# Kernel tuning notes

Hardware: AMD Instinct MI355X
Metric: run time of the kernel (lower is better)

Reference implementation:

```python
import jax, jax.numpy as jnp
from jax import lax
import numpy as np

DN = ('NHWC', 'HWIO', 'NHWC')


def setup_inputs() -> dict:
    key = jax.random.key(0)
    ks = jax.random.split(key, 4)
    B, T, H, W, Cin, Cout, K = 4, 16, 64, 64, 32, 64, 3
    x = jax.random.normal(ks[0], (B, T, H, W, Cin), dtype=jnp.float32)
    kernel = jax.random.normal(ks[1], (K, K, Cin, 4 * Cout), dtype=jnp.float32) * 0.05
    rec_kernel = jax.random.normal(ks[2], (K, K, Cout, 4 * Cout), dtype=jnp.float32) * 0.05
    bias = jnp.zeros((4 * Cout,), dtype=jnp.float32)
    gamma = jnp.ones((Cout,), dtype=jnp.float32)
    beta = jnp.zeros((Cout,), dtype=jnp.float32)
    moving_mean = jnp.zeros((Cout,), dtype=jnp.float32)
    moving_var = jnp.ones((Cout,), dtype=jnp.float32)
    return dict(x=x, kernel=kernel, rec_kernel=rec_kernel, bias=bias,
                gamma=gamma, beta=beta, moving_mean=moving_mean, moving_var=moving_var)


def _hard_sigmoid(z):
    # Keras hard_sigmoid: clip(0.2*x + 0.5, 0, 1)
    return jnp.clip(0.2 * z + 0.5, 0.0, 1.0)


def _conv(x, w):
    return lax.conv_general_dilated(x, w, (1, 1), 'SAME', dimension_numbers=DN)


def reference(x, kernel, rec_kernel, bias, gamma, beta, moving_mean, moving_var):
    B, T, H, W, Cin = x.shape
    Cout = rec_kernel.shape[2]
    # Precompute input-to-gate convs for all timesteps at once: (B*T,H,W,4C)
    gx = _conv(x.reshape(B * T, H, W, Cin), kernel) + bias
    gx = gx.reshape(B, T, H, W, 4 * Cout).transpose(1, 0, 2, 3, 4)  # (T,B,H,W,4C)

    def step(carry, gxt):
        h, c = carry
        g = gxt + _conv(h, rec_kernel)  # (B,H,W,4C)
        i, f, cc, o = jnp.split(g, 4, axis=-1)  # Keras gate order i,f,c,o
        i = _hard_sigmoid(i)
        f = _hard_sigmoid(f)
        c = f * c + i * jnp.tanh(cc)
        h = _hard_sigmoid(o) * jnp.tanh(c)
        return (h, c), h

    h0 = jnp.zeros((B, H, W, Cout), dtype=x.dtype)
    c0 = jnp.zeros((B, H, W, Cout), dtype=x.dtype)
    _, hs = lax.scan(step, (h0, c0), gx)  # (T,B,H,W,C)
    y = hs.transpose(1, 0, 2, 3, 4)  # (B,T,H,W,C)
    # BatchNorm, inference mode (training=False), eps=1e-3
    inv = gamma * lax.rsqrt(moving_var + 1e-3)
    return y * inv + (beta - moving_mean * inv)
```

## Files before the change

kernel.cpp:

```cpp
#include <hip/hip_runtime.h>
#include <math.h>

#define B_ 4
#define T_ 16
#define H_ 64
#define W_ 64
#define CIN 32
#define CO 64
#define NG 256
#define PXS 40

typedef __attribute__((ext_vector_type(8))) short bf16x8;
typedef __attribute__((ext_vector_type(4))) float f32x4;

__device__ __forceinline__ float hsig(float z) {
    return fminf(1.f, fmaxf(0.f, 0.2f * z + 0.5f));
}

__device__ __forceinline__ float ftanh(float x) {
    float e = __builtin_amdgcn_exp2f(x * 2.8853900817779268f);
    return 1.f - 2.f * __builtin_amdgcn_rcpf(e + 1.f);
}

__device__ __forceinline__ unsigned short f2bf(float f) {
    union { float f; unsigned u; } v; v.f = f;
    unsigned r = v.u + 0x7FFFu + ((v.u >> 16) & 1u);
    return (unsigned short)(r >> 16);
}

__global__ void transform_weights(const float* __restrict__ wk,
                                  const float* __restrict__ wr,
                                  unsigned short* __restrict__ wkT,
                                  unsigned short* __restrict__ wrT)
{
    int i = blockIdx.x * 256 + threadIdx.x;
    if (i < 9 * 256 * 32) {
        int k = i & 31, n = (i >> 5) & 255, kpos = i >> 13;
        wkT[i] = f2bf(wk[(kpos * 32 + k) * 256 + n]);
    }
    if (i < 9 * 2 * 256 * 32) {
        int k = i & 31, n = (i >> 5) & 255, q = (i >> 13) & 1, kpos = i >> 14;
        wrT[i] = f2bf(wr[(kpos * 64 + q * 32 + k) * 256 + n]);
    }
}

template<bool FIRST>
__global__ __launch_bounds__(512, 2)
void convlstm_step(const float* __restrict__ x,
                   const unsigned short* __restrict__ wkT,
                   const unsigned short* __restrict__ wrT,
                   const float* __restrict__ bias,
                   const float* __restrict__ gamma,
                   const float* __restrict__ beta,
                   const float* __restrict__ mean,
                   const float* __restrict__ var,
                   const unsigned short* __restrict__ hin,
                   unsigned short* __restrict__ hout,
                   float* __restrict__ cbuf,
                   float* __restrict__ out,
                   int t)
{
    __shared__ __align__(16) unsigned short sx[6 * 18 * PXS];
    __shared__ __align__(16) unsigned short sh[2][6 * 18 * PXS];
    __shared__ __align__(16) float axx[4 * 4 * 4 * 16 * 20];

    const int tid = threadIdx.x;
    const int wv = tid >> 6, lane = tid & 63;
    const int ln = lane & 15, kg = lane >> 4;
    const bool hwave = (wv < 4);
    const int sl = wv & 3;

    const int bi = blockIdx.x;
    const int b = bi >> 6, tile = bi & 63;
    const int oy = (tile >> 2) * 4;
    const int ox = (tile & 3) * 16;

    if (!hwave) {
#pragma unroll
        for (int i = 0; i < 2; ++i) {
            int e = (tid - 256) + i * 256;
            if (e < 432) {
                int c8 = e & 3, p = e >> 2;
                int row = p / 18, col = p - row * 18;
                int gy = oy - 1 + row, gx = ox - 1 + col;
                float4 v0 = make_float4(0.f, 0.f, 0.f, 0.f), v1 = v0;
                if ((unsigned)gy < (unsigned)H_ && (unsigned)gx < (unsigned)W_) {
                    const float* p32 = &x[((((size_t)b * T_ + t) * H_ + gy) * W_ + gx) * CIN + c8 * 8];
                    v0 = *(const float4*)p32; v1 = *(const float4*)(p32 + 4);
                }
                unsigned short* d = &sx[(row * 18 + col) * PXS + c8 * 8];
                d[0] = f2bf(v0.x); d[1] = f2bf(v0.y); d[2] = f2bf(v0.z); d[3] = f2bf(v0.w);
                d[4] = f2bf(v1.x); d[5] = f2bf(v1.y); d[6] = f2bf(v1.z); d[7] = f2bf(v1.w);
            }
        }
    } else if (!FIRST) {
#pragma unroll
        for (int i = 0; i < 4; ++i) {
            int e = tid + i * 256;
            if (e < 864) {
                int o = e & 7, p = e >> 3;
                int row = p / 18, col = p - row * 18;
                int gy = oy - 1 + row, gx = ox - 1 + col;
                uint4 v = make_uint4(0u, 0u, 0u, 0u);
                if ((unsigned)gy < (unsigned)H_ && (unsigned)gx < (unsigned)W_)
                    v = *(const uint4*)&hin[(((size_t)b * H_ + gy) * W_ + gx) * CO + o * 8];
                int q = o >> 2, s4 = o & 3;
                *(uint4*)&sh[q][(row * 18 + col) * PXS + s4 * 8] = v;
            }
        }
    }
    __syncthreads();

    f32x4 acc[4][4];
#pragma unroll
    for (int g = 0; g < 4; ++g)
#pragma unroll
        for (int r = 0; r < 4; ++r) acc[g][r] = (f32x4){0.f, 0.f, 0.f, 0.f};

    const int nbase = sl * 16 + ln;

    if (!hwave) {
        const unsigned short* wkp = wkT + (size_t)nbase * 32 + kg * 8;
        bf16x8 bx[4];
#pragma unroll
        for (int g = 0; g < 4; ++g)
            bx[g] = *(const bf16x8*)(wkp + (size_t)(g * 64) * 32);
#pragma unroll
        for (int kpos = 0; kpos < 9; ++kpos) {
            const int ky = kpos / 3, kx = kpos - ky * 3;
            bf16x8 nbx[4];
            if (kpos < 8) {
#pragma unroll
                for (int g = 0; g < 4; ++g)
                    nbx[g] = *(const bf16x8*)(wkp + (size_t)((kpos + 1) * 256 + g * 64) * 32);
            }
            bf16x8 a[4];
#pragma unroll
            for (int r = 0; r < 4; ++r)
                a[r] = *(const bf16x8*)&sx[((r + ky) * 18 + ln + kx) * PXS + kg * 8];
#pragma unroll
            for (int g = 0; g < 4; ++g)
#pragma unroll
                for (int r = 0; r < 4; ++r)
                    acc[g][r] = __builtin_amdgcn_mfma_f32_16x16x32_bf16(a[r], bx[g], acc[g][r], 0, 0, 0);
            if (kpos < 8) {
#pragma unroll
                for (int g = 0; g < 4; ++g) bx[g] = nbx[g];
            }
        }
    } else if (!FIRST) {
        const unsigned short* wrp = wrT + (size_t)nbase * 32 + kg * 8;
        bf16x8 bh[2][4];
#pragma unroll
        for (int q = 0; q < 2; ++q)
#pragma unroll
            for (int g = 0; g < 4; ++g)
                bh[q][g] = *(const bf16x8*)(wrp + (size_t)(q * 256 + g * 64) * 32);
#pragma unroll
        for (int kpos = 0; kpos < 9; ++kpos) {
            const int ky = kpos / 3, kx = kpos - ky * 3;
            bf16x8 nbh[2][4];
            if (kpos < 8) {
#pragma unroll
                for (int q = 0; q < 2; ++q)
#pragma unroll
                    for (int g = 0; g < 4; ++g)
                        nbh[q][g] = *(const bf16x8*)(wrp + (size_t)(((kpos + 1) * 2 + q) * 256 + g * 64) * 32);
            }
#pragma unroll
            for (int q = 0; q < 2; ++q) {
                bf16x8 a[4];
#pragma unroll
                for (int r = 0; r < 4; ++r)
                    a[r] = *(const bf16x8*)&sh[q][((r + ky) * 18 + ln + kx) * PXS + kg * 8];
#pragma unroll
                for (int g = 0; g < 4; ++g)
#pragma unroll
                    for (int r = 0; r < 4; ++r)
                        acc[g][r] = __builtin_amdgcn_mfma_f32_16x16x32_bf16(a[r], bh[q][g], acc[g][r], 0, 0, 0);
            }
            if (kpos < 8) {
#pragma unroll
                for (int q = 0; q < 2; ++q)
#pragma unroll
                    for (int g = 0; g < 4; ++g) bh[q][g] = nbh[q][g];
            }
        }
    }

    if (!hwave) {
#pragma unroll
        for (int g = 0; g < 4; ++g)
#pragma unroll
            for (int r = 0; r < 4; ++r)
                *(f32x4*)&axx[((((sl * 4 + g) * 4 + r) * 16) + ln) * 20 + kg * 4] = acc[g][r];
    }
    __syncthreads();
    if (!hwave) return;

#pragma unroll
    for (int g = 0; g < 4; ++g)
#pragma unroll
        for (int r = 0; r < 4; ++r) {
            f32x4 v = *(const f32x4*)&axx[((((sl * 4 + g) * 4 + r) * 16) + ln) * 20 + kg * 4];
            acc[g][r] += v;
        }

    const int ch = sl * 16 + ln;
    const float bi0 = bias[ch], bi1 = bias[64 + ch], bi2 = bias[128 + ch], bi3 = bias[192 + ch];
    const float inv = gamma[ch] * rsqrtf(var[ch] + 1e-3f);
    const float shift = beta[ch] - mean[ch] * inv;

    float cprev[4][4];
    if (!FIRST) {
#pragma unroll
        for (int r = 0; r < 4; ++r)
#pragma unroll
            for (int reg = 0; reg < 4; ++reg) {
                size_t pix = ((size_t)b * H_ + oy + r) * W_ + (ox + kg * 4 + reg);
                cprev[r][reg] = cbuf[pix * CO + ch];
            }
    } else {
#pragma unroll
        for (int r = 0; r < 4; ++r)
#pragma unroll
            for (int reg = 0; reg < 4; ++reg) cprev[r][reg] = 0.f;
    }

#pragma unroll
    for (int r = 0; r < 4; ++r) {
        const int gy = oy + r;
#pragma unroll
        for (int reg = 0; reg < 4; ++reg) {
            const int gx = ox + kg * 4 + reg;
            size_t pix = ((size_t)b * H_ + gy) * W_ + gx;
            float ig = hsig(acc[0][r][reg] + bi0);
            float fg = hsig(acc[1][r][reg] + bi1);
            float cg = ftanh(acc[2][r][reg] + bi2);
            float og = hsig(acc[3][r][reg] + bi3);
            float cv = fg * cprev[r][reg] + ig * cg;
            float hv = og * ftanh(cv);
            cbuf[pix * CO + ch] = cv;
            hout[pix * CO + ch] = f2bf(hv);
            out[((((size_t)b * T_ + t) * H_ + gy) * W_ + gx) * CO + ch] = hv * inv + shift;
        }
    }
}

extern "C" void kernel_launch(void* const* d_in, const int* in_sizes, int n_in,
                              void* d_out, int out_size, void* d_ws, size_t ws_size,
                              hipStream_t stream)
{
    (void)in_sizes; (void)n_in; (void)out_size; (void)ws_size;
    const float* x     = (const float*)d_in[0];
    const float* wk    = (const float*)d_in[1];
    const float* wr    = (const float*)d_in[2];
    const float* bias  = (const float*)d_in[3];
    const float* gamma = (const float*)d_in[4];
    const float* beta  = (const float*)d_in[5];
    const float* mean  = (const float*)d_in[6];
    const float* var   = (const float*)d_in[7];
    float* out = (float*)d_out;

    const size_t plane = (size_t)B_ * H_ * W_ * CO;
    unsigned short* h0 = (unsigned short*)d_ws;
    unsigned short* h1 = h0 + plane;
    float* cb = (float*)(h1 + plane);
    unsigned short* wkT = (unsigned short*)(cb + plane);
    unsigned short* wrT = wkT + 9 * 256 * 32;

    transform_weights<<<576, 256, 0, stream>>>(wk, wr, wkT, wrT);

    for (int t = 0; t < T_; ++t) {
        const unsigned short* hin = (t & 1) ? h0 : h1;
        unsigned short* houtp     = (t & 1) ? h1 : h0;
        if (t == 0)
            convlstm_step<true><<<256, 512, 0, stream>>>(x, wkT, wrT, bias, gamma, beta, mean, var,
                                                         hin, houtp, cb, out, t);
        else
            convlstm_step<false><<<256, 512, 0, stream>>>(x, wkT, wrT, bias, gamma, beta, mean, var,
                                                          hin, houtp, cb, out, t);
    }
}
```

Baseline: 308.8 us.

## Rebalance MFMA work between x-wave and h-wave, prefetch cell state, nontemporal stores

The recurrent conv's second channel half is split across the two wave groups: the x-conv waves now also handle kernel positions 0-4 of the h-conv's second 32-channel half, and the h-waves keep positions 5-8. This evens out MFMA counts between the waves so they reach the barrier at about the same time. Bias, batchnorm params and the previous cell state are now loaded before the MFMA loop so their latency is hidden behind compute. MFMA blocks are wrapped in s_setprio, and the c and output stores become nontemporal, which trades cache residency of cbuf for reduced write traffic.

```diff
diff --git a/kernel.cpp b/kernel.cpp
--- a/kernel.cpp
+++ b/kernel.cpp
@@ -111,79 +111,145 @@
     }
     __syncthreads();
 
+    const int nbase = sl * 16 + ln;
+    const int ch = nbase;
+
+    float bi0 = 0.f, bi1 = 0.f, bi2 = 0.f, bi3 = 0.f, inv = 0.f, shift = 0.f;
+    float cprev[4][4];
+    if (hwave) {
+        bi0 = bias[ch]; bi1 = bias[64 + ch]; bi2 = bias[128 + ch]; bi3 = bias[192 + ch];
+        inv = gamma[ch] * rsqrtf(var[ch] + 1e-3f);
+        shift = beta[ch] - mean[ch] * inv;
+        if (!FIRST) {
+#pragma unroll
+            for (int r = 0; r < 4; ++r)
+#pragma unroll
+                for (int reg = 0; reg < 4; ++reg) {
+                    size_t pix = ((size_t)b * H_ + oy + r) * W_ + (ox + kg * 4 + reg);
+                    cprev[r][reg] = cbuf[pix * CO + ch];
+                }
+        } else {
+#pragma unroll
+            for (int r = 0; r < 4; ++r)
+#pragma unroll
+                for (int reg = 0; reg < 4; ++reg) cprev[r][reg] = 0.f;
+        }
+    }
+
     f32x4 acc[4][4];
 #pragma unroll
     for (int g = 0; g < 4; ++g)
 #pragma unroll
         for (int r = 0; r < 4; ++r) acc[g][r] = (f32x4){0.f, 0.f, 0.f, 0.f};
-
-    const int nbase = sl * 16 + ln;
 
     if (!hwave) {
         const unsigned short* wkp = wkT + (size_t)nbase * 32 + kg * 8;
-        bf16x8 bx[4];
+        const unsigned short* wrp = wrT + (size_t)nbase * 32 + kg * 8;
+        bf16x8 bx[4], bq[4];
 #pragma unroll
         for (int g = 0; g < 4; ++g)
             bx[g] = *(const bf16x8*)(wkp + (size_t)(g * 64) * 32);
+        if (!FIRST) {
+#pragma unroll
+            for (int g = 0; g < 4; ++g)
+                bq[g] = *(const bf16x8*)(wrp + (size_t)(1 * 256 + g * 64) * 32);
+        }
 #pragma unroll
         for (int kpos = 0; kpos < 9; ++kpos) {
             const int ky = kpos / 3, kx = kpos - ky * 3;
-            bf16x8 nbx[4];
+            bf16x8 nbx[4], nbq[4];
             if (kpos < 8) {
 #pragma unroll
                 for (int g = 0; g < 4; ++g)
                     nbx[g] = *(const bf16x8*)(wkp + (size_t)((kpos + 1) * 256 + g * 64) * 32);
             }
+            if (!FIRST && kpos < 4) {
+#pragma unroll
+                for (int g = 0; g < 4; ++g)
+                    nbq[g] = *(const bf16x8*)(wrp + (size_t)(((kpos + 1) * 2 + 1) * 256 + g * 64) * 32);
+            }
             bf16x8 a[4];
 #pragma unroll
             for (int r = 0; r < 4; ++r)
                 a[r] = *(const bf16x8*)&sx[((r + ky) * 18 + ln + kx) * PXS + kg * 8];
+            __builtin_amdgcn_s_setprio(1);
 #pragma unroll
             for (int g = 0; g < 4; ++g)
 #pragma unroll
                 for (int r = 0; r < 4; ++r)
                     acc[g][r] = __builtin_amdgcn_mfma_f32_16x16x32_bf16(a[r], bx[g], acc[g][r], 0, 0, 0);
+            __builtin_amdgcn_s_setprio(0);
+            if (!FIRST && kpos < 5) {
+#pragma unroll
+                for (int r = 0; r < 4; ++r)
+                    a[r] = *(const bf16x8*)&sh[1][((r + ky) * 18 + ln + kx) * PXS + kg * 8];
+                __builtin_amdgcn_s_setprio(1);
+#pragma unroll
+                for (int g = 0; g < 4; ++g)
+#pragma unroll
+                    for (int r = 0; r < 4; ++r)
+                        acc[g][r] = __builtin_amdgcn_mfma_f32_16x16x32_bf16(a[r], bq[g], acc[g][r], 0, 0, 0);
+                __builtin_amdgcn_s_setprio(0);
+            }
             if (kpos < 8) {
 #pragma unroll
                 for (int g = 0; g < 4; ++g) bx[g] = nbx[g];
+            }
+            if (!FIRST && kpos < 4) {
+#pragma unroll
+                for (int g = 0; g < 4; ++g) bq[g] = nbq[g];
             }
         }
     } else if (!FIRST) {
         const unsigned short* wrp = wrT + (size_t)nbase * 32 + kg * 8;
-        bf16x8 bh[2][4];
-#pragma unroll
-        for (int q = 0; q < 2; ++q)
-#pragma unroll
-            for (int g = 0; g < 4; ++g)
-                bh[q][g] = *(const bf16x8*)(wrp + (size_t)(q * 256 + g * 64) * 32);
+        bf16x8 bq0[4], bq1[4];
+#pragma unroll
+        for (int g = 0; g < 4; ++g)
+            bq0[g] = *(const bf16x8*)(wrp + (size_t)(g * 64) * 32);
 #pragma unroll
         for (int kpos = 0; kpos < 9; ++kpos) {
             const int ky = kpos / 3, kx = kpos - ky * 3;
-            bf16x8 nbh[2][4];
+            bf16x8 nbq0[4], nbq1[4];
             if (kpos < 8) {
 #pragma unroll
-                for (int q = 0; q < 2; ++q)
-#pragma unroll
-                    for (int g = 0; g < 4; ++g)
-                        nbh[q][g] = *(const bf16x8*)(wrp + (size_t)(((kpos + 1) * 2 + q) * 256 + g * 64) * 32);
-            }
-#pragma unroll
-            for (int q = 0; q < 2; ++q) {
-                bf16x8 a[4];
+                for (int g = 0; g < 4; ++g)
+                    nbq0[g] = *(const bf16x8*)(wrp + (size_t)((kpos + 1) * 2 * 256 + g * 64) * 32);
+            }
+            if (kpos >= 4 && kpos < 8) {
+#pragma unroll
+                for (int g = 0; g < 4; ++g)
+                    nbq1[g] = *(const bf16x8*)(wrp + (size_t)(((kpos + 1) * 2 + 1) * 256 + g * 64) * 32);
+            }
+            bf16x8 a[4];
+#pragma unroll
+            for (int r = 0; r < 4; ++r)
+                a[r] = *(const bf16x8*)&sh[0][((r + ky) * 18 + ln + kx) * PXS + kg * 8];
+            __builtin_amdgcn_s_setprio(1);
+#pragma unroll
+            for (int g = 0; g < 4; ++g)
 #pragma unroll
                 for (int r = 0; r < 4; ++r)
-                    a[r] = *(const bf16x8*)&sh[q][((r + ky) * 18 + ln + kx) * PXS + kg * 8];
+                    acc[g][r] = __builtin_amdgcn_mfma_f32_16x16x32_bf16(a[r], bq0[g], acc[g][r], 0, 0, 0);
+            __builtin_amdgcn_s_setprio(0);
+            if (kpos >= 5) {
+#pragma unroll
+                for (int r = 0; r < 4; ++r)
+                    a[r] = *(const bf16x8*)&sh[1][((r + ky) * 18 + ln + kx) * PXS + kg * 8];
+                __builtin_amdgcn_s_setprio(1);
 #pragma unroll
                 for (int g = 0; g < 4; ++g)
 #pragma unroll
                     for (int r = 0; r < 4; ++r)
-                        acc[g][r] = __builtin_amdgcn_mfma_f32_16x16x32_bf16(a[r], bh[q][g], acc[g][r], 0, 0, 0);
+                        acc[g][r] = __builtin_amdgcn_mfma_f32_16x16x32_bf16(a[r], bq1[g], acc[g][r], 0, 0, 0);
+                __builtin_amdgcn_s_setprio(0);
             }
             if (kpos < 8) {
 #pragma unroll
-                for (int q = 0; q < 2; ++q)
-#pragma unroll
-                    for (int g = 0; g < 4; ++g) bh[q][g] = nbh[q][g];
+                for (int g = 0; g < 4; ++g) bq0[g] = nbq0[g];
+            }
+            if (kpos >= 4 && kpos < 8) {
+#pragma unroll
+                for (int g = 0; g < 4; ++g) bq1[g] = nbq1[g];
             }
         }
     }
@@ -205,27 +271,6 @@
             f32x4 v = *(const f32x4*)&axx[((((sl * 4 + g) * 4 + r) * 16) + ln) * 20 + kg * 4];
             acc[g][r] += v;
         }
-
-    const int ch = sl * 16 + ln;
-    const float bi0 = bias[ch], bi1 = bias[64 + ch], bi2 = bias[128 + ch], bi3 = bias[192 + ch];
-    const float inv = gamma[ch] * rsqrtf(var[ch] + 1e-3f);
-    const float shift = beta[ch] - mean[ch] * inv;
-
-    float cprev[4][4];
-    if (!FIRST) {
-#pragma unroll
-        for (int r = 0; r < 4; ++r)
-#pragma unroll
-            for (int reg = 0; reg < 4; ++reg) {
-                size_t pix = ((size_t)b * H_ + oy + r) * W_ + (ox + kg * 4 + reg);
-                cprev[r][reg] = cbuf[pix * CO + ch];
-            }
-    } else {
-#pragma unroll
-        for (int r = 0; r < 4; ++r)
-#pragma unroll
-            for (int reg = 0; reg < 4; ++reg) cprev[r][reg] = 0.f;
-    }
 
 #pragma unroll
     for (int r = 0; r < 4; ++r) {
@@ -240,9 +285,10 @@
             float og = hsig(acc[3][r][reg] + bi3);
             float cv = fg * cprev[r][reg] + ig * cg;
             float hv = og * ftanh(cv);
-            cbuf[pix * CO + ch] = cv;
+            __builtin_nontemporal_store(cv, &cbuf[pix * CO + ch]);
             hout[pix * CO + ch] = f2bf(hv);
-            out[((((size_t)b * T_ + t) * H_ + gy) * W_ + gx) * CO + ch] = hv * inv + shift;
+            __builtin_nontemporal_store(hv * inv + shift,
+                &out[((((size_t)b * T_ + t) * H_ + gy) * W_ + gx) * CO + ch]);
         }
     }
 }
```

New measurement: 288.5 us. -6.6%, faster.

## Balance MFMA work between x and h waves and split gate epilogue

Applied to the files above, without the earlier changes.

Rebalances the convolution work so the x-wave also takes part of the recurrent conv (second channel half), giving 14 vs 13 chunks instead of 9 vs 18. Both waves now exchange partial sums through LDS and each runs the gate epilogue for half the rows, so no wave idles after the barrier. Weight loads use a deeper 3-ahead register pipeline, MFMA blocks are wrapped in s_setprio, and the c-state and output stores are nontemporal. The cost is higher register pressure from the deeper pipeline, and the h-wave now depends on partial sums from the x-wave for every row.

```diff
diff --git a/kernel.cpp b/kernel.cpp
--- a/kernel.cpp
+++ b/kernel.cpp
@@ -109,140 +109,137 @@
             }
         }
     }
-    __syncthreads();
-
-    f32x4 acc[4][4];
-#pragma unroll
-    for (int g = 0; g < 4; ++g)
-#pragma unroll
-        for (int r = 0; r < 4; ++r) acc[g][r] = (f32x4){0.f, 0.f, 0.f, 0.f};
 
     const int nbase = sl * 16 + ln;
-
-    if (!hwave) {
-        const unsigned short* wkp = wkT + (size_t)nbase * 32 + kg * 8;
-        bf16x8 bx[4];
-#pragma unroll
-        for (int g = 0; g < 4; ++g)
-            bx[g] = *(const bf16x8*)(wkp + (size_t)(g * 64) * 32);
-#pragma unroll
-        for (int kpos = 0; kpos < 9; ++kpos) {
-            const int ky = kpos / 3, kx = kpos - ky * 3;
-            bf16x8 nbx[4];
-            if (kpos < 8) {
-#pragma unroll
-                for (int g = 0; g < 4; ++g)
-                    nbx[g] = *(const bf16x8*)(wkp + (size_t)((kpos + 1) * 256 + g * 64) * 32);
-            }
-            bf16x8 a[4];
-#pragma unroll
-            for (int r = 0; r < 4; ++r)
-                a[r] = *(const bf16x8*)&sx[((r + ky) * 18 + ln + kx) * PXS + kg * 8];
-#pragma unroll
-            for (int g = 0; g < 4; ++g)
-#pragma unroll
-                for (int r = 0; r < 4; ++r)
-                    acc[g][r] = __builtin_amdgcn_mfma_f32_16x16x32_bf16(a[r], bx[g], acc[g][r], 0, 0, 0);
-            if (kpos < 8) {
-#pragma unroll
-                for (int g = 0; g < 4; ++g) bx[g] = nbx[g];
-            }
-        }
-    } else if (!FIRST) {
-        const unsigned short* wrp = wrT + (size_t)nbase * 32 + kg * 8;
-        bf16x8 bh[2][4];
-#pragma unroll
-        for (int q = 0; q < 2; ++q)
-#pragma unroll
-            for (int g = 0; g < 4; ++g)
-                bh[q][g] = *(const bf16x8*)(wrp + (size_t)(q * 256 + g * 64) * 32);
-#pragma unroll
-        for (int kpos = 0; kpos < 9; ++kpos) {
-            const int ky = kpos / 3, kx = kpos - ky * 3;
-            bf16x8 nbh[2][4];
-            if (kpos < 8) {
-#pragma unroll
-                for (int q = 0; q < 2; ++q)
-#pragma unroll
-                    for (int g = 0; g < 4; ++g)
-                        nbh[q][g] = *(const bf16x8*)(wrp + (size_t)(((kpos + 1) * 2 + q) * 256 + g * 64) * 32);
-            }
-#pragma unroll
-            for (int q = 0; q < 2; ++q) {
-                bf16x8 a[4];
-#pragma unroll
-                for (int r = 0; r < 4; ++r)
-                    a[r] = *(const bf16x8*)&sh[q][((r + ky) * 18 + ln + kx) * PXS + kg * 8];
-#pragma unroll
-                for (int g = 0; g < 4; ++g)
-#pragma unroll
-                    for (int r = 0; r < 4; ++r)
-                        acc[g][r] = __builtin_amdgcn_mfma_f32_16x16x32_bf16(a[r], bh[q][g], acc[g][r], 0, 0, 0);
-            }
-            if (kpos < 8) {
-#pragma unroll
-                for (int q = 0; q < 2; ++q)
-#pragma unroll
-                    for (int g = 0; g < 4; ++g) bh[q][g] = nbh[q][g];
-            }
-        }
-    }
-
-    if (!hwave) {
-#pragma unroll
-        for (int g = 0; g < 4; ++g)
-#pragma unroll
-            for (int r = 0; r < 4; ++r)
-                *(f32x4*)&axx[((((sl * 4 + g) * 4 + r) * 16) + ln) * 20 + kg * 4] = acc[g][r];
-    }
-    __syncthreads();
-    if (!hwave) return;
-
-#pragma unroll
-    for (int g = 0; g < 4; ++g)
-#pragma unroll
-        for (int r = 0; r < 4; ++r) {
-            f32x4 v = *(const f32x4*)&axx[((((sl * 4 + g) * 4 + r) * 16) + ln) * 20 + kg * 4];
-            acc[g][r] += v;
-        }
-
-    const int ch = sl * 16 + ln;
+    const int ch = nbase;
+    const unsigned short* wkp = wkT + (size_t)nbase * 32 + kg * 8;
+    const unsigned short* wrp = wrT + (size_t)nbase * 32 + kg * 8;
+
+    const int rbase = hwave ? 0 : 2;
     const float bi0 = bias[ch], bi1 = bias[64 + ch], bi2 = bias[128 + ch], bi3 = bias[192 + ch];
     const float inv = gamma[ch] * rsqrtf(var[ch] + 1e-3f);
     const float shift = beta[ch] - mean[ch] * inv;
-
-    float cprev[4][4];
+    float cprev[2][4];
     if (!FIRST) {
 #pragma unroll
-        for (int r = 0; r < 4; ++r)
+        for (int rr = 0; rr < 2; ++rr)
 #pragma unroll
             for (int reg = 0; reg < 4; ++reg) {
-                size_t pix = ((size_t)b * H_ + oy + r) * W_ + (ox + kg * 4 + reg);
-                cprev[r][reg] = cbuf[pix * CO + ch];
+                size_t pix = ((size_t)b * H_ + oy + rbase + rr) * W_ + (ox + kg * 4 + reg);
+                cprev[rr][reg] = cbuf[pix * CO + ch];
             }
     } else {
 #pragma unroll
-        for (int r = 0; r < 4; ++r)
-#pragma unroll
-            for (int reg = 0; reg < 4; ++reg) cprev[r][reg] = 0.f;
-    }
-
-#pragma unroll
-    for (int r = 0; r < 4; ++r) {
+        for (int rr = 0; rr < 2; ++rr)
+#pragma unroll
+            for (int reg = 0; reg < 4; ++reg) cprev[rr][reg] = 0.f;
+    }
+
+    __syncthreads();
+
+    f32x4 acc[4][4];
+#pragma unroll
+    for (int g = 0; g < 4; ++g)
+#pragma unroll
+        for (int r = 0; r < 4; ++r) acc[g][r] = (f32x4){0.f, 0.f, 0.f, 0.f};
+
+#define LOADW_X(dst, i) {                                                        \
+    const unsigned short* wp_ = (i < 9) ? (wkp + (size_t)(i) * 8192)             \
+                                        : (wrp + (size_t)(((i) - 9) * 2 + 1) * 8192); \
+    dst[0] = *(const bf16x8*)(wp_);                                              \
+    dst[1] = *(const bf16x8*)(wp_ + 2048);                                       \
+    dst[2] = *(const bf16x8*)(wp_ + 4096);                                       \
+    dst[3] = *(const bf16x8*)(wp_ + 6144); }
+#define LOADW_H(dst, i) {                                                        \
+    const unsigned short* wp_ = (i < 9) ? (wrp + (size_t)((i) * 2) * 8192)       \
+                                        : (wrp + (size_t)(((i) - 4) * 2 + 1) * 8192); \
+    dst[0] = *(const bf16x8*)(wp_);                                              \
+    dst[1] = *(const bf16x8*)(wp_ + 2048);                                       \
+    dst[2] = *(const bf16x8*)(wp_ + 4096);                                       \
+    dst[3] = *(const bf16x8*)(wp_ + 6144); }
+
+    if (!hwave) {
+        constexpr int NC = FIRST ? 9 : 14;
+        bf16x8 pipe[4][4];
+#pragma unroll
+        for (int i = 0; i < 3; ++i) { if (i < NC) LOADW_X(pipe[i], i); }
+#pragma unroll
+        for (int i = 0; i < NC; ++i) {
+            if (i + 3 < NC) LOADW_X(pipe[(i + 3) & 3], (i + 3));
+            const int kq = (i < 9) ? i : i - 9;
+            const int ky = kq / 3, kx = kq - ky * 3;
+            const unsigned short* sb = (i < 9) ? sx : sh[1];
+            bf16x8 a[4];
+#pragma unroll
+            for (int r = 0; r < 4; ++r)
+                a[r] = *(const bf16x8*)&sb[((r + ky) * 18 + ln + kx) * PXS + kg * 8];
+            __builtin_amdgcn_s_setprio(1);
+#pragma unroll
+            for (int g = 0; g < 4; ++g)
+#pragma unroll
+                for (int r = 0; r < 4; ++r)
+                    acc[g][r] = __builtin_amdgcn_mfma_f32_16x16x32_bf16(a[r], pipe[i & 3][g], acc[g][r], 0, 0, 0);
+            __builtin_amdgcn_s_setprio(0);
+        }
+    } else if (!FIRST) {
+        constexpr int NC = 13;
+        bf16x8 pipe[4][4];
+#pragma unroll
+        for (int i = 0; i < 3; ++i) { LOADW_H(pipe[i], i); }
+#pragma unroll
+        for (int i = 0; i < NC; ++i) {
+            if (i + 3 < NC) LOADW_H(pipe[(i + 3) & 3], (i + 3));
+            const int kq = (i < 9) ? i : i - 4;
+            const int ky = kq / 3, kx = kq - ky * 3;
+            const unsigned short* sb = (i < 9) ? sh[0] : sh[1];
+            bf16x8 a[4];
+#pragma unroll
+            for (int r = 0; r < 4; ++r)
+                a[r] = *(const bf16x8*)&sb[((r + ky) * 18 + ln + kx) * PXS + kg * 8];
+            __builtin_amdgcn_s_setprio(1);
+#pragma unroll
+            for (int g = 0; g < 4; ++g)
+#pragma unroll
+                for (int r = 0; r < 4; ++r)
+                    acc[g][r] = __builtin_amdgcn_mfma_f32_16x16x32_bf16(a[r], pipe[i & 3][g], acc[g][r], 0, 0, 0);
+            __builtin_amdgcn_s_setprio(0);
+        }
+    }
+
+    {
+        const int pb = hwave ? 2 : 0;
+#pragma unroll
+        for (int g = 0; g < 4; ++g)
+#pragma unroll
+            for (int rr = 0; rr < 2; ++rr)
+                *(f32x4*)&axx[((((sl * 4 + g) * 4 + (pb + rr)) * 16) + ln) * 20 + kg * 4] = acc[g][pb + rr];
+    }
+    __syncthreads();
+
+#pragma unroll
+    for (int rr = 0; rr < 2; ++rr) {
+        const int r = rbase + rr;
         const int gy = oy + r;
+        f32x4 av[4];
+#pragma unroll
+        for (int g = 0; g < 4; ++g) {
+            f32x4 v = *(const f32x4*)&axx[((((sl * 4 + g) * 4 + r) * 16) + ln) * 20 + kg * 4];
+            av[g] = acc[g][r] + v;
+        }
 #pragma unroll
         for (int reg = 0; reg < 4; ++reg) {
             const int gx = ox + kg * 4 + reg;
             size_t pix = ((size_t)b * H_ + gy) * W_ + gx;
-            float ig = hsig(acc[0][r][reg] + bi0);
-            float fg = hsig(acc[1][r][reg] + bi1);
-            float cg = ftanh(acc[2][r][reg] + bi2);
-            float og = hsig(acc[3][r][reg] + bi3);
-            float cv = fg * cprev[r][reg] + ig * cg;
+            float ig = hsig(av[0][reg] + bi0);
+            float fg = hsig(av[1][reg] + bi1);
+            float cg = ftanh(av[2][reg] + bi2);
+            float og = hsig(av[3][reg] + bi3);
+            float cv = fg * cprev[rr][reg] + ig * cg;
             float hv = og * ftanh(cv);
-            cbuf[pix * CO + ch] = cv;
+            __builtin_nontemporal_store(cv, &cbuf[pix * CO + ch]);
             hout[pix * CO + ch] = f2bf(hv);
-            out[((((size_t)b * T_ + t) * H_ + gy) * W_ + gx) * CO + ch] = hv * inv + shift;
+            __builtin_nontemporal_store(hv * inv + shift,
+                &out[((((size_t)b * T_ + t) * H_ + gy) * W_ + gx) * CO + ch]);
         }
     }
 }
```

Result: slower. 910.2 us (+194.7%).
